# Performance work log

Measured on AMD Instinct MI355X. Metric: run time of the kernel, lower is better.

## Reference

```python
import jax, jax.numpy as jnp
import numpy as np

EPS = 1e-5
N = 384
CZ = 128  # pair channels (c_z)
CH = 128  # hidden channels (c_hidden)


def _layer_norm(x, w, b):
    m = jnp.mean(x, axis=-1, keepdims=True)
    v = jnp.mean(jnp.square(x - m), axis=-1, keepdims=True)
    return (x - m) * jax.lax.rsqrt(v + EPS) * w + b


def setup_inputs() -> dict:
    key = jax.random.key(0)
    ks = jax.random.split(key, 8)
    s = 0.02  # weight init scale
    return {
        "z": jax.random.normal(ks[0], (1, N, N, CZ), jnp.float32),
        "ln_in_w": jnp.ones((2, CZ), jnp.float32),
        "ln_in_b": jnp.zeros((2, CZ), jnp.float32),
        "w_ag": jax.random.normal(ks[1], (2, CZ, CH), jnp.float32) * s,
        "b_ag": jnp.zeros((2, CH), jnp.float32),
        "w_ap": jax.random.normal(ks[2], (2, CZ, CH), jnp.float32) * s,
        "b_ap": jnp.zeros((2, CH), jnp.float32),
        "w_bg": jax.random.normal(ks[3], (2, CZ, CH), jnp.float32) * s,
        "b_bg": jnp.zeros((2, CH), jnp.float32),
        "w_bp": jax.random.normal(ks[4], (2, CZ, CH), jnp.float32) * s,
        "b_bp": jnp.zeros((2, CH), jnp.float32),
        "ln_out_w": jnp.ones((2, CH), jnp.float32),
        "ln_out_b": jnp.zeros((2, CH), jnp.float32),
        "w_z": jax.random.normal(ks[5], (2, CH, CZ), jnp.float32) * s,
        "b_z": jnp.zeros((2, CZ), jnp.float32),
        "w_g": jax.random.normal(ks[6], (2, CZ, CZ), jnp.float32) * s,
        "b_g": jnp.zeros((2, CZ), jnp.float32),
    }


def _tri_mul(z, outgoing, ln_in_w, ln_in_b, w_ag, b_ag, w_ap, b_ap,
             w_bg, b_bg, w_bp, b_bp, ln_out_w, ln_out_b, w_z, b_z, w_g, b_g):
    zn = _layer_norm(z, ln_in_w, ln_in_b)                      # [1,N,N,CZ]
    a = jax.nn.sigmoid(zn @ w_ag + b_ag) * (zn @ w_ap + b_ap)  # [1,N,N,CH]
    b = jax.nn.sigmoid(zn @ w_bg + b_bg) * (zn @ w_bp + b_bp)  # [1,N,N,CH]
    if outgoing:
        # p[i,k,c] = sum_j a[i,j,c] * b[k,j,c]
        p = jnp.einsum('bijc,bkjc->bikc', a, b)
    else:
        # p[i,k,c] = sum_j a[j,i,c] * b[j,k,c]
        p = jnp.einsum('bjic,bjkc->bikc', a, b)
    p = _layer_norm(p, ln_out_w, ln_out_b) @ w_z + b_z         # [1,N,N,CZ]
    g = jax.nn.sigmoid(zn @ w_g + b_g)
    return p * g


def reference(z, ln_in_w, ln_in_b, w_ag, b_ag, w_ap, b_ap, w_bg, b_bg,
              w_bp, b_bp, ln_out_w, ln_out_b, w_z, b_z, w_g, b_g):
    # idx 0: TriMulOut (outgoing=True), idx 1: TriMulIn (outgoing=False)
    for idx, outgoing in enumerate((True, False)):
        z = z + _tri_mul(z, outgoing,
                         ln_in_w[idx], ln_in_b[idx],
                         w_ag[idx], b_ag[idx], w_ap[idx], b_ap[idx],
                         w_bg[idx], b_bg[idx], w_bp[idx], b_bp[idx],
                         ln_out_w[idx], ln_out_b[idx],
                         w_z[idx], b_z[idx], w_g[idx], b_g[idx])
    return z
```

## Files before the change

### kernel.cpp

```cpp
#include <hip/hip_runtime.h>


constexpr int NS = 384;
constexpr int NN = NS * NS;

using bf16x8 = __attribute__((ext_vector_type(8))) __bf16;
using f32x4  = __attribute__((ext_vector_type(4))) float;

__device__ inline void load16_to_lds(const __bf16* g, __bf16* lds) {
  auto* gp = reinterpret_cast<const __attribute__((address_space(1))) unsigned int*>(
      reinterpret_cast<uintptr_t>(g));
  auto* lp = reinterpret_cast<__attribute__((address_space(3))) unsigned int*>(
      reinterpret_cast<uintptr_t>(lds));
  __builtin_amdgcn_global_load_lds(gp, lp, 16, 0, 0);
}

__global__ __launch_bounds__(256) void prep_weights(
    const float* __restrict__ w_ag, const float* __restrict__ w_ap,
    const float* __restrict__ w_bg, const float* __restrict__ w_bp,
    const float* __restrict__ w_g,  const float* __restrict__ w_z,
    __bf16* __restrict__ wsw)
{
  int gid  = blockIdx.x * 256 + threadIdx.x;
  int mat  = gid >> 11;
  int slot = gid & 2047;
  int lane = slot & 63;
  int tb   = (slot >> 6) & 7;
  int s    = slot >> 9;
  int pass = mat / 6, which = mat % 6;
  const float* W;
  switch (which) {
    case 0: W = w_ag; break; case 1: W = w_ap; break; case 2: W = w_bg; break;
    case 3: W = w_bp; break; case 4: W = w_g;  break; default: W = w_z;
  }
  W += pass * 16384;
  int n0 = tb * 16 + (lane & 15);
  int k0 = s * 32 + (lane >> 4) * 8;
  __bf16* dst = wsw + ((size_t)mat * 2048 + slot) * 8;
#pragma unroll
  for (int j = 0; j < 8; ++j) dst[j] = (__bf16)W[(k0 + j) * 128 + n0];
}

__global__ __launch_bounds__(256) void proj_kernel(
    const float* __restrict__ zsrc, const float* __restrict__ lnw, const float* __restrict__ lnb,
    const __bf16* __restrict__ wsw5,
    const float* __restrict__ bag, const float* __restrict__ bap,
    const float* __restrict__ bbg, const float* __restrict__ bbp, const float* __restrict__ bgg,
    __bf16* __restrict__ a_t, __bf16* __restrict__ b_t, __bf16* __restrict__ g_out, int mode)
{
  __shared__ __bf16 zn[64][136];
  int tid = threadIdx.x;
  int rb = 0, r2 = 0;
  size_t pstart = 0;
  if (mode == 0) pstart = (size_t)blockIdx.x * 64;
  else { rb = blockIdx.x / NS; r2 = blockIdx.x % NS; }

  {
    int row = tid >> 2, q = tid & 3;
    size_t zoff = (mode == 0) ? (pstart + row) * 128
                              : ((size_t)(64 * rb + row) * NS + r2) * 128;
    const float4* zp = (const float4*)(zsrc + zoff) + q * 8;
    float4 v[8];
#pragma unroll
    for (int u = 0; u < 8; ++u) v[u] = zp[u];
    float s1 = 0.f, s2 = 0.f;
#pragma unroll
    for (int u = 0; u < 8; ++u) {
      float4 t = v[u];
      s1 += t.x + t.y + t.z + t.w;
      s2 += t.x * t.x + t.y * t.y + t.z * t.z + t.w * t.w;
    }
    s1 += __shfl_xor(s1, 1); s2 += __shfl_xor(s2, 1);
    s1 += __shfl_xor(s1, 2); s2 += __shfl_xor(s2, 2);
    float mean = s1 * (1.0f / 128.0f);
    float var  = s2 * (1.0f / 128.0f) - mean * mean;
    float rstd = rsqrtf(var + 1e-5f);
#pragma unroll
    for (int u = 0; u < 8; ++u) {
      int c0 = q * 32 + u * 4;
      float4 t  = v[u];
      float4 w4 = *(const float4*)(lnw + c0);
      float4 b4 = *(const float4*)(lnb + c0);
      zn[row][c0 + 0] = (__bf16)((t.x - mean) * rstd * w4.x + b4.x);
      zn[row][c0 + 1] = (__bf16)((t.y - mean) * rstd * w4.y + b4.y);
      zn[row][c0 + 2] = (__bf16)((t.z - mean) * rstd * w4.z + b4.z);
      zn[row][c0 + 3] = (__bf16)((t.w - mean) * rstd * w4.w + b4.w);
    }
  }
  __syncthreads();

  const int wv = tid >> 6;
  const int lane = tid & 63;
  const int lm = lane & 15;
  const int lq = lane >> 4;
  const size_t wposbase = (mode == 0) ? pstart : ((size_t)r2 * NS + 64 * rb);

  bf16x8 znf[4][4];
#pragma unroll
  for (int nt = 0; nt < 4; ++nt)
#pragma unroll
    for (int s = 0; s < 4; ++s)
      znf[nt][s] = *(const bf16x8*)(&zn[16 * nt + lm][32 * s + 8 * lq]);

#pragma unroll
  for (int grp = 0; grp < 3; ++grp) {
    const __bf16* wA;
    const __bf16* wB = nullptr;
    const float* pbA;
    const float* pbB = nullptr;
    __bf16* dst = nullptr;
    if (grp == 0)      { wA = wsw5;             wB = wsw5 + 16384;   pbA = bag; pbB = bap; dst = a_t; }
    else if (grp == 1) { wA = wsw5 + 2 * 16384; wB = wsw5 + 3 * 16384; pbA = bbg; pbB = bbp; dst = b_t; }
    else               { wA = wsw5 + 4 * 16384; pbA = bgg; }

#pragma unroll
    for (int mbi = 0; mbi < 2; ++mbi) {
      const int mb = 2 * wv + mbi;
      bf16x8 fA[4], fB[4];
#pragma unroll
      for (int s = 0; s < 4; ++s) {
        fA[s] = *(const bf16x8*)(wA + ((size_t)((s * 8 + mb) * 64 + lane)) * 8);
        if (grp < 2) fB[s] = *(const bf16x8*)(wB + ((size_t)((s * 8 + mb) * 64 + lane)) * 8);
      }
      if (grp < 2) {
        float biasA[4], biasB[4];
#pragma unroll
        for (int r = 0; r < 4; ++r) {
          int cc = 16 * mb + 4 * lq + r;
          biasA[r] = pbA[cc];
          biasB[r] = pbB[cc];
        }
#pragma unroll
        for (int nt = 0; nt < 4; ++nt) {
          f32x4 acc0 = {0.f, 0.f, 0.f, 0.f}, acc1 = {0.f, 0.f, 0.f, 0.f};
#pragma unroll
          for (int s = 0; s < 4; ++s) {
            acc0 = __builtin_amdgcn_mfma_f32_16x16x32_bf16(fA[s], znf[nt][s], acc0, 0, 0, 0);
            acc1 = __builtin_amdgcn_mfma_f32_16x16x32_bf16(fB[s], znf[nt][s], acc1, 0, 0, 0);
          }
          size_t wp = wposbase + 16 * nt + lm;
#pragma unroll
          for (int r = 0; r < 4; ++r) {
            int cc = 16 * mb + 4 * lq + r;
            float xg = acc0[r] + biasA[r];
            float xp = acc1[r] + biasB[r];
            float val = xp / (1.0f + __expf(-xg));
            dst[(size_t)cc * NN + wp] = (__bf16)val;
          }
        }
      } else {
        float biasG = pbA[16 * mb + lm];
#pragma unroll
        for (int nt = 0; nt < 4; ++nt) {
          f32x4 acc = {0.f, 0.f, 0.f, 0.f};
#pragma unroll
          for (int s = 0; s < 4; ++s)
            acc = __builtin_amdgcn_mfma_f32_16x16x32_bf16(znf[nt][s], fA[s], acc, 0, 0, 0);
          int cc = 16 * mb + lm;
#pragma unroll
          for (int r = 0; r < 4; ++r) {
            int pos = 16 * nt + 4 * lq + r;
            size_t gp = (mode == 0) ? (pstart + pos) * 128
                                    : ((size_t)(64 * rb + pos) * NS + r2) * 128;
            float val = 1.0f / (1.0f + __expf(-(acc[r] + biasG)));
            g_out[gp + cc] = (__bf16)val;
          }
        }
      }
    }
  }
}

__global__ __launch_bounds__(256) void tri_kernel(
    const __bf16* __restrict__ a_t, const __bf16* __restrict__ b_t, __bf16* __restrict__ p_t)
{
  __shared__ __bf16 As[128 * 64];
  __shared__ __bf16 Bs[128 * 64];
  int c  = blockIdx.z;
  int i0 = blockIdx.x * 128, k0 = blockIdx.y * 128;
  const __bf16* Ab = a_t + (size_t)c * NN;
  const __bf16* Bb = b_t + (size_t)c * NN;
  int tid = threadIdx.x, wv = tid >> 6, lane = tid & 63;
  int lm = lane & 15, lq = lane >> 4;
  int lrow = lane >> 3;
  int lsl  = lane & 7;
  int lch  = lsl ^ lrow;
  f32x4 acc[4][4];
#pragma unroll
  for (int mi = 0; mi < 4; ++mi)
#pragma unroll
    for (int ni = 0; ni < 4; ++ni) acc[mi][ni] = {0.f, 0.f, 0.f, 0.f};
  const int rowA_half = 64 * (wv & 1), colB_half = 64 * (wv >> 1);

  for (int kk = 0; kk < 384; kk += 64) {
    __syncthreads();
#pragma unroll
    for (int v = 0; v < 4; ++v) {
      int rgrp = 4 * wv + v;
      int r = 8 * rgrp + lrow;
      load16_to_lds(Ab + (size_t)(i0 + r) * NS + kk + lch * 8, As + rgrp * 512);
      load16_to_lds(Bb + (size_t)(k0 + r) * NS + kk + lch * 8, Bs + rgrp * 512);
    }
    __syncthreads();
#pragma unroll
    for (int s = 0; s < 2; ++s) {
      bf16x8 bfr[4], afr[4];
#pragma unroll
      for (int ni = 0; ni < 4; ++ni)
        bfr[ni] = *(const bf16x8*)(Bs + (colB_half + 16 * ni + lm) * 64 +
                                   ((4 * s + lq) ^ (lm & 7)) * 8);
#pragma unroll
      for (int mi = 0; mi < 4; ++mi)
        afr[mi] = *(const bf16x8*)(As + (rowA_half + 16 * mi + lm) * 64 +
                                   ((4 * s + lq) ^ (lm & 7)) * 8);
#pragma unroll
      for (int mi = 0; mi < 4; ++mi)
#pragma unroll
        for (int ni = 0; ni < 4; ++ni)
          acc[mi][ni] = __builtin_amdgcn_mfma_f32_16x16x32_bf16(afr[mi], bfr[ni], acc[mi][ni], 0, 0, 0);
    }
  }
#pragma unroll
  for (int mi = 0; mi < 4; ++mi)
#pragma unroll
    for (int ni = 0; ni < 4; ++ni)
#pragma unroll
      for (int r = 0; r < 4; ++r) {
        int row = i0 + rowA_half + 16 * mi + 4 * lq + r;
        int col = k0 + colB_half + 16 * ni + lm;
        p_t[(size_t)c * NN + (size_t)row * NS + col] = (__bf16)acc[mi][ni][r];
      }
}

__global__ __launch_bounds__(256) void out_kernel(
    const __bf16* __restrict__ p_t, const __bf16* __restrict__ g_in,
    const float* __restrict__ z_in, float* __restrict__ z_out,
    const float* __restrict__ lnw, const float* __restrict__ lnb,
    const __bf16* __restrict__ wz, const float* __restrict__ bz)
{
  __shared__ __bf16 pl[64][136];
  int tid = threadIdx.x;
  size_t base = (size_t)blockIdx.x * 64;

  {
    int c2 = tid >> 1, hf = tid & 1;
    const __bf16* src = p_t + (size_t)c2 * NN + base + hf * 32;
    bf16x8 v0 = ((const bf16x8*)src)[0];
    bf16x8 v1 = ((const bf16x8*)src)[1];
    bf16x8 v2 = ((const bf16x8*)src)[2];
    bf16x8 v3 = ((const bf16x8*)src)[3];
#pragma unroll
    for (int j = 0; j < 8; ++j) pl[hf * 32 + j][c2] = v0[j];
#pragma unroll
    for (int j = 0; j < 8; ++j) pl[hf * 32 + 8 + j][c2] = v1[j];
#pragma unroll
    for (int j = 0; j < 8; ++j) pl[hf * 32 + 16 + j][c2] = v2[j];
#pragma unroll
    for (int j = 0; j < 8; ++j) pl[hf * 32 + 24 + j][c2] = v3[j];
  }
  __syncthreads();

  {
    int row = tid >> 2, q = tid & 3;
    bf16x8 pv[4];
#pragma unroll
    for (int s = 0; s < 4; ++s) pv[s] = *(const bf16x8*)(&pl[row][q * 32 + 8 * s]);
    float s1 = 0.f, s2 = 0.f;
#pragma unroll
    for (int s = 0; s < 4; ++s)
#pragma unroll
      for (int j = 0; j < 8; ++j) { float f = (float)pv[s][j]; s1 += f; s2 += f * f; }
    s1 += __shfl_xor(s1, 1); s2 += __shfl_xor(s2, 1);
    s1 += __shfl_xor(s1, 2); s2 += __shfl_xor(s2, 2);
    float mean = s1 * (1.0f / 128.0f);
    float var  = s2 * (1.0f / 128.0f) - mean * mean;
    float rstd = rsqrtf(var + 1e-5f);
#pragma unroll
    for (int s = 0; s < 4; ++s) {
#pragma unroll
      for (int j = 0; j < 8; ++j) {
        int cc = q * 32 + 8 * s + j;
        float f = ((float)pv[s][j] - mean) * rstd * lnw[cc] + lnb[cc];
        pv[s][j] = (__bf16)f;
      }
      *(bf16x8*)(&pl[row][q * 32 + 8 * s]) = pv[s];
    }
  }
  __syncthreads();

  int wv = tid >> 6, lane = tid & 63, lm = lane & 15, lq = lane >> 4;
  bf16x8 wzf[2][4];
  float bzv[2];
#pragma unroll
  for (int nbi = 0; nbi < 2; ++nbi) {
    int nb = 2 * wv + nbi;
    bzv[nbi] = bz[16 * nb + lm];
#pragma unroll
    for (int s = 0; s < 4; ++s)
      wzf[nbi][s] = *(const bf16x8*)(wz + ((size_t)((s * 8 + nb) * 64 + lane)) * 8);
  }
#pragma unroll
  for (int mt = 0; mt < 4; ++mt) {
    bf16x8 af[4];
#pragma unroll
    for (int s = 0; s < 4; ++s)
      af[s] = *(const bf16x8*)(&pl[16 * mt + lm][32 * s + 8 * lq]);
#pragma unroll
    for (int nbi = 0; nbi < 2; ++nbi) {
      f32x4 acc = {0.f, 0.f, 0.f, 0.f};
#pragma unroll
      for (int s = 0; s < 4; ++s)
        acc = __builtin_amdgcn_mfma_f32_16x16x32_bf16(af[s], wzf[nbi][s], acc, 0, 0, 0);
      int cz = 16 * (2 * wv + nbi) + lm;
#pragma unroll
      for (int r = 0; r < 4; ++r) {
        int pos = 16 * mt + 4 * lq + r;
        size_t idx = (base + pos) * 128 + cz;
        float gv  = (float)g_in[idx];
        float res = (acc[r] + bzv[nbi]) * gv + z_in[idx];
        z_out[idx] = res;
      }
    }
  }
}

extern "C" void kernel_launch(void* const* d_in, const int* in_sizes, int n_in,
                              void* d_out, int out_size, void* d_ws, size_t ws_size,
                              hipStream_t stream) {
  (void)in_sizes; (void)n_in; (void)out_size; (void)ws_size;
  const float* z        = (const float*)d_in[0];
  const float* ln_in_w  = (const float*)d_in[1];
  const float* ln_in_b  = (const float*)d_in[2];
  const float* w_ag     = (const float*)d_in[3];
  const float* b_ag     = (const float*)d_in[4];
  const float* w_ap     = (const float*)d_in[5];
  const float* b_ap     = (const float*)d_in[6];
  const float* w_bg     = (const float*)d_in[7];
  const float* b_bg     = (const float*)d_in[8];
  const float* w_bp     = (const float*)d_in[9];
  const float* b_bp     = (const float*)d_in[10];
  const float* ln_out_w = (const float*)d_in[11];
  const float* ln_out_b = (const float*)d_in[12];
  const float* w_z      = (const float*)d_in[13];
  const float* b_z      = (const float*)d_in[14];
  const float* w_g      = (const float*)d_in[15];
  const float* b_g      = (const float*)d_in[16];
  float* out = (float*)d_out;

  __bf16* wsw = (__bf16*)d_ws;
  __bf16* a_t = wsw + 12 * 16384;
  __bf16* b_t = a_t + (size_t)NN * 128;
  __bf16* g_b = b_t + (size_t)NN * 128;
  __bf16* p_t = g_b + (size_t)NN * 128;

  prep_weights<<<96, 256, 0, stream>>>(w_ag, w_ap, w_bg, w_bp, w_g, w_z, wsw);

  for (int idx = 0; idx < 2; ++idx) {
    const float* zsrc = (idx == 0) ? z : out;
    const __bf16* wsw5 = wsw + (size_t)idx * 6 * 16384;
    proj_kernel<<<2304, 256, 0, stream>>>(
        zsrc, ln_in_w + idx * 128, ln_in_b + idx * 128, wsw5,
        b_ag + idx * 128, b_ap + idx * 128, b_bg + idx * 128, b_bp + idx * 128,
        b_g + idx * 128, a_t, b_t, g_b, idx);
    tri_kernel<<<dim3(3, 3, 128), 256, 0, stream>>>(a_t, b_t, p_t);
    out_kernel<<<2304, 256, 0, stream>>>(
        p_t, g_b, zsrc, out, ln_out_w + idx * 128, ln_out_b + idx * 128,
        wsw5 + 5 * 16384, b_z + idx * 128);
  }
}
```

Baseline: 461.4 us.

## Split input layernorm into own kernel and restage projection outputs through LDS

New measurement: 543.0 us. 1.18x slower.

```diff
diff --git a/kernel.cpp b/kernel.cpp
--- a/kernel.cpp
+++ b/kernel.cpp
@@ -13,6 +13,11 @@
   auto* lp = reinterpret_cast<__attribute__((address_space(3))) unsigned int*>(
       reinterpret_cast<uintptr_t>(lds));
   __builtin_amdgcn_global_load_lds(gp, lp, 16, 0, 0);
+}
+
+__device__ inline float sigmoidf_fast(float x) {
+  float e = __expf(-x);
+  return __builtin_amdgcn_rcpf(1.0f + e);
 }
 
 __global__ __launch_bounds__(256) void prep_weights(
@@ -41,132 +46,186 @@
   for (int j = 0; j < 8; ++j) dst[j] = (__bf16)W[(k0 + j) * 128 + n0];
 }
 
-__global__ __launch_bounds__(256) void proj_kernel(
+__global__ __launch_bounds__(256) void ln_kernel(
     const float* __restrict__ zsrc, const float* __restrict__ lnw, const float* __restrict__ lnb,
-    const __bf16* __restrict__ wsw5,
+    __bf16* __restrict__ zn, int mode)
+{
+  int tid = threadIdx.x;
+  int row = tid >> 2, q = tid & 3;
+  size_t zoff, qidx;
+  if (mode == 0) { qidx = (size_t)blockIdx.x * 64 + row; zoff = qidx * 128; }
+  else {
+    int i = blockIdx.x / 6;
+    int j = (blockIdx.x % 6) * 64 + row;
+    zoff = ((size_t)j * NS + i) * 128;
+    qidx = (size_t)i * NS + j;
+  }
+  const float4* zp = (const float4*)(zsrc + zoff) + q * 8;
+  float4 v[8];
+#pragma unroll
+  for (int u = 0; u < 8; ++u) v[u] = zp[u];
+  float s1 = 0.f, s2 = 0.f;
+#pragma unroll
+  for (int u = 0; u < 8; ++u) {
+    float4 t = v[u];
+    s1 += t.x + t.y + t.z + t.w;
+    s2 += t.x * t.x + t.y * t.y + t.z * t.z + t.w * t.w;
+  }
+  s1 += __shfl_xor(s1, 1); s2 += __shfl_xor(s2, 1);
+  s1 += __shfl_xor(s1, 2); s2 += __shfl_xor(s2, 2);
+  float mean = s1 * (1.0f / 128.0f);
+  float var  = s2 * (1.0f / 128.0f) - mean * mean;
+  float rstd = rsqrtf(var + 1e-5f);
+  bf16x8 o[4];
+#pragma unroll
+  for (int u = 0; u < 8; ++u) {
+    int c0 = q * 32 + u * 4;
+    float4 t  = v[u];
+    float4 w4 = *(const float4*)(lnw + c0);
+    float4 b4 = *(const float4*)(lnb + c0);
+    o[u >> 1][(u & 1) * 4 + 0] = (__bf16)((t.x - mean) * rstd * w4.x + b4.x);
+    o[u >> 1][(u & 1) * 4 + 1] = (__bf16)((t.y - mean) * rstd * w4.y + b4.y);
+    o[u >> 1][(u & 1) * 4 + 2] = (__bf16)((t.z - mean) * rstd * w4.z + b4.z);
+    o[u >> 1][(u & 1) * 4 + 3] = (__bf16)((t.w - mean) * rstd * w4.w + b4.w);
+  }
+  __bf16* dst = zn + qidx * 128 + q * 32;
+#pragma unroll
+  for (int u = 0; u < 4; ++u) *(bf16x8*)(dst + u * 8) = o[u];
+}
+
+__global__ __launch_bounds__(256, 2) void proj2_kernel(
+    const __bf16* __restrict__ zn, const __bf16* __restrict__ wsw5,
     const float* __restrict__ bag, const float* __restrict__ bap,
-    const float* __restrict__ bbg, const float* __restrict__ bbp, const float* __restrict__ bgg,
-    __bf16* __restrict__ a_t, __bf16* __restrict__ b_t, __bf16* __restrict__ g_out, int mode)
+    const float* __restrict__ bbg, const float* __restrict__ bbp,
+    const float* __restrict__ bgg,
+    __bf16* __restrict__ a_t, __bf16* __restrict__ b_t, __bf16* __restrict__ g_out,
+    int mode)
 {
-  __shared__ __bf16 zn[64][136];
-  int tid = threadIdx.x;
-  int rb = 0, r2 = 0;
-  size_t pstart = 0;
-  if (mode == 0) pstart = (size_t)blockIdx.x * 64;
-  else { rb = blockIdx.x / NS; r2 = blockIdx.x % NS; }
+  __shared__ __bf16 znlds[128 * 128];
+  __shared__ __bf16 alds[128 * 128];
+
+  const int tid = threadIdx.x;
+  const int wv = tid >> 6, lane = tid & 63;
+  const int lm = lane & 15, lq = lane >> 4;
+  const int prod = blockIdx.y;
+  const bool twomat = (prod != 2);
+  const __bf16* wbase = wsw5 + (size_t)prod * 2 * 16384;
+  const size_t pbase = (size_t)blockIdx.x * 128;
 
   {
-    int row = tid >> 2, q = tid & 3;
-    size_t zoff = (mode == 0) ? (pstart + row) * 128
-                              : ((size_t)(64 * rb + row) * NS + r2) * 128;
-    const float4* zp = (const float4*)(zsrc + zoff) + q * 8;
-    float4 v[8];
-#pragma unroll
-    for (int u = 0; u < 8; ++u) v[u] = zp[u];
-    float s1 = 0.f, s2 = 0.f;
-#pragma unroll
-    for (int u = 0; u < 8; ++u) {
-      float4 t = v[u];
-      s1 += t.x + t.y + t.z + t.w;
-      s2 += t.x * t.x + t.y * t.y + t.z * t.z + t.w * t.w;
-    }
-    s1 += __shfl_xor(s1, 1); s2 += __shfl_xor(s2, 1);
-    s1 += __shfl_xor(s1, 2); s2 += __shfl_xor(s2, 2);
-    float mean = s1 * (1.0f / 128.0f);
-    float var  = s2 * (1.0f / 128.0f) - mean * mean;
-    float rstd = rsqrtf(var + 1e-5f);
-#pragma unroll
-    for (int u = 0; u < 8; ++u) {
-      int c0 = q * 32 + u * 4;
-      float4 t  = v[u];
-      float4 w4 = *(const float4*)(lnw + c0);
-      float4 b4 = *(const float4*)(lnb + c0);
-      zn[row][c0 + 0] = (__bf16)((t.x - mean) * rstd * w4.x + b4.x);
-      zn[row][c0 + 1] = (__bf16)((t.y - mean) * rstd * w4.y + b4.y);
-      zn[row][c0 + 2] = (__bf16)((t.z - mean) * rstd * w4.z + b4.z);
-      zn[row][c0 + 3] = (__bf16)((t.w - mean) * rstd * w4.w + b4.w);
-    }
-  }
+    const __bf16* zsrc = zn + pbase * 128;
+    int lrow = lane >> 4, lsl = lane & 15;
+#pragma unroll
+    for (int t = 0; t < 8; ++t) {
+      int rbase = (wv * 8 + t) * 4;
+      int row = rbase + lrow;
+      int chunk = lsl ^ (row & 15);
+      load16_to_lds(zsrc + (size_t)row * 128 + chunk * 8, znlds + rbase * 128);
+    }
+  }
+
+  const int n0 = 2 * wv;
+  bf16x8 wf[2][2][4];
+#pragma unroll
+  for (int n2 = 0; n2 < 2; ++n2)
+#pragma unroll
+    for (int s = 0; s < 4; ++s) {
+      wf[n2][0][s] = *(const bf16x8*)(wbase + ((size_t)((s * 8 + n0 + n2) * 64 + lane)) * 8);
+      if (twomat)
+        wf[n2][1][s] = *(const bf16x8*)(wbase + 16384 + ((size_t)((s * 8 + n0 + n2) * 64 + lane)) * 8);
+    }
+  const float* pbA = (prod == 0) ? bag : (prod == 1) ? bbg : bgg;
+  const float* pbB = (prod == 0) ? bap : bbp;
+  float bA[2], bB[2];
+#pragma unroll
+  for (int n2 = 0; n2 < 2; ++n2) {
+    bA[n2] = pbA[(n0 + n2) * 16 + lm];
+    bB[n2] = twomat ? pbB[(n0 + n2) * 16 + lm] : 0.f;
+  }
+
+  f32x4 acc[8][2][2];
+#pragma unroll
+  for (int m = 0; m < 8; ++m)
+#pragma unroll
+    for (int n2 = 0; n2 < 2; ++n2)
+#pragma unroll
+      for (int mt = 0; mt < 2; ++mt) acc[m][n2][mt] = {0.f, 0.f, 0.f, 0.f};
+
   __syncthreads();
 
-  const int wv = tid >> 6;
-  const int lane = tid & 63;
-  const int lm = lane & 15;
-  const int lq = lane >> 4;
-  const size_t wposbase = (mode == 0) ? pstart : ((size_t)r2 * NS + 64 * rb);
-
-  bf16x8 znf[4][4];
-#pragma unroll
-  for (int nt = 0; nt < 4; ++nt)
+#pragma unroll
+  for (int m = 0; m < 8; ++m) {
+    bf16x8 zf[4];
+#pragma unroll
+    for (int s = 0; s < 4; ++s) {
+      int slot = (4 * s + lq) ^ lm;
+      zf[s] = *(const bf16x8*)(znlds + (m * 16 + lm) * 128 + slot * 8);
+    }
 #pragma unroll
     for (int s = 0; s < 4; ++s)
-      znf[nt][s] = *(const bf16x8*)(&zn[16 * nt + lm][32 * s + 8 * lq]);
-
-#pragma unroll
-  for (int grp = 0; grp < 3; ++grp) {
-    const __bf16* wA;
-    const __bf16* wB = nullptr;
-    const float* pbA;
-    const float* pbB = nullptr;
-    __bf16* dst = nullptr;
-    if (grp == 0)      { wA = wsw5;             wB = wsw5 + 16384;   pbA = bag; pbB = bap; dst = a_t; }
-    else if (grp == 1) { wA = wsw5 + 2 * 16384; wB = wsw5 + 3 * 16384; pbA = bbg; pbB = bbp; dst = b_t; }
-    else               { wA = wsw5 + 4 * 16384; pbA = bgg; }
-
-#pragma unroll
-    for (int mbi = 0; mbi < 2; ++mbi) {
-      const int mb = 2 * wv + mbi;
-      bf16x8 fA[4], fB[4];
-#pragma unroll
-      for (int s = 0; s < 4; ++s) {
-        fA[s] = *(const bf16x8*)(wA + ((size_t)((s * 8 + mb) * 64 + lane)) * 8);
-        if (grp < 2) fB[s] = *(const bf16x8*)(wB + ((size_t)((s * 8 + mb) * 64 + lane)) * 8);
-      }
-      if (grp < 2) {
-        float biasA[4], biasB[4];
+#pragma unroll
+      for (int n2 = 0; n2 < 2; ++n2) {
+        acc[m][n2][0] = __builtin_amdgcn_mfma_f32_16x16x32_bf16(zf[s], wf[n2][0][s], acc[m][n2][0], 0, 0, 0);
+        if (twomat)
+          acc[m][n2][1] = __builtin_amdgcn_mfma_f32_16x16x32_bf16(zf[s], wf[n2][1][s], acc[m][n2][1], 0, 0, 0);
+      }
+  }
+
+  if (prod < 2) {
+#pragma unroll
+    for (int m = 0; m < 8; ++m)
+#pragma unroll
+      for (int n2 = 0; n2 < 2; ++n2) {
+        int c = (n0 + n2) * 16 + lm;
+#pragma unroll
+        for (int rr = 0; rr < 2; ++rr) {
+          int pos = m * 16 + 4 * lq + 2 * rr;
+          float g0 = acc[m][n2][0][2 * rr]     + bA[n2];
+          float g1 = acc[m][n2][0][2 * rr + 1] + bA[n2];
+          float p0 = acc[m][n2][1][2 * rr]     + bB[n2];
+          float p1 = acc[m][n2][1][2 * rr + 1] + bB[n2];
+          union { __bf16 h[2]; unsigned u; } pk;
+          pk.h[0] = (__bf16)(p0 * sigmoidf_fast(g0));
+          pk.h[1] = (__bf16)(p1 * sigmoidf_fast(g1));
+          int addr = c * 128 + (((pos >> 3) ^ (c & 15)) << 3) + (pos & 7);
+          *(unsigned*)(&alds[addr]) = pk.u;
+        }
+      }
+    __syncthreads();
+    __bf16* outp = (prod == 0) ? a_t : b_t;
+    int c = tid & 127, half = tid >> 7;
+    __bf16* dst = outp + (size_t)c * NN + pbase;
+#pragma unroll
+    for (int jj = 0; jj < 8; ++jj) {
+      int j = half * 8 + jj;
+      bf16x8 vv = *(const bf16x8*)(&alds[c * 128 + ((j ^ (c & 15)) << 3)]);
+      *(bf16x8*)(dst + j * 8) = vv;
+    }
+  } else {
+#pragma unroll
+    for (int m = 0; m < 8; ++m)
+#pragma unroll
+      for (int n2 = 0; n2 < 2; ++n2) {
+        int c = (n0 + n2) * 16 + lm;
 #pragma unroll
         for (int r = 0; r < 4; ++r) {
-          int cc = 16 * mb + 4 * lq + r;
-          biasA[r] = pbA[cc];
-          biasB[r] = pbB[cc];
+          int pos = m * 16 + 4 * lq + r;
+          float gv = sigmoidf_fast(acc[m][n2][0][r] + bA[n2]);
+          int addr = pos * 128 + (((c >> 3) ^ (pos & 15)) << 3) + (c & 7);
+          alds[addr] = (__bf16)gv;
         }
-#pragma unroll
-        for (int nt = 0; nt < 4; ++nt) {
-          f32x4 acc0 = {0.f, 0.f, 0.f, 0.f}, acc1 = {0.f, 0.f, 0.f, 0.f};
-#pragma unroll
-          for (int s = 0; s < 4; ++s) {
-            acc0 = __builtin_amdgcn_mfma_f32_16x16x32_bf16(fA[s], znf[nt][s], acc0, 0, 0, 0);
-            acc1 = __builtin_amdgcn_mfma_f32_16x16x32_bf16(fB[s], znf[nt][s], acc1, 0, 0, 0);
-          }
-          size_t wp = wposbase + 16 * nt + lm;
-#pragma unroll
-          for (int r = 0; r < 4; ++r) {
-            int cc = 16 * mb + 4 * lq + r;
-            float xg = acc0[r] + biasA[r];
-            float xp = acc1[r] + biasB[r];
-            float val = xp / (1.0f + __expf(-xg));
-            dst[(size_t)cc * NN + wp] = (__bf16)val;
-          }
-        }
-      } else {
-        float biasG = pbA[16 * mb + lm];
-#pragma unroll
-        for (int nt = 0; nt < 4; ++nt) {
-          f32x4 acc = {0.f, 0.f, 0.f, 0.f};
-#pragma unroll
-          for (int s = 0; s < 4; ++s)
-            acc = __builtin_amdgcn_mfma_f32_16x16x32_bf16(znf[nt][s], fA[s], acc, 0, 0, 0);
-          int cc = 16 * mb + lm;
-#pragma unroll
-          for (int r = 0; r < 4; ++r) {
-            int pos = 16 * nt + 4 * lq + r;
-            size_t gp = (mode == 0) ? (pstart + pos) * 128
-                                    : ((size_t)(64 * rb + pos) * NS + r2) * 128;
-            float val = 1.0f / (1.0f + __expf(-(acc[r] + biasG)));
-            g_out[gp + cc] = (__bf16)val;
-          }
-        }
-      }
+      }
+    __syncthreads();
+    int pos = tid & 127, half = tid >> 7;
+    size_t q = pbase + pos;
+    size_t gp;
+    if (mode == 0) gp = q;
+    else { int i = (int)(q / NS); int j = (int)(q % NS); gp = (size_t)j * NS + i; }
+    __bf16* dst = g_out + gp * 128;
+#pragma unroll
+    for (int jj = 0; jj < 8; ++jj) {
+      int j = half * 8 + jj;
+      *(bf16x8*)(dst + j * 8) = *(const bf16x8*)(&alds[pos * 128 + ((j ^ (pos & 15)) << 3)]);
     }
   }
 }
@@ -347,24 +406,26 @@
   const float* b_g      = (const float*)d_in[16];
   float* out = (float*)d_out;
 
-  __bf16* wsw = (__bf16*)d_ws;
-  __bf16* a_t = wsw + 12 * 16384;
-  __bf16* b_t = a_t + (size_t)NN * 128;
-  __bf16* g_b = b_t + (size_t)NN * 128;
-  __bf16* p_t = g_b + (size_t)NN * 128;
+  __bf16* wsw  = (__bf16*)d_ws;
+  __bf16* a_t  = wsw + 12 * 16384;
+  __bf16* b_t  = a_t + (size_t)NN * 128;
+  __bf16* g_b  = b_t + (size_t)NN * 128;
+  __bf16* znpt = g_b + (size_t)NN * 128;
 
   prep_weights<<<96, 256, 0, stream>>>(w_ag, w_ap, w_bg, w_bp, w_g, w_z, wsw);
 
   for (int idx = 0; idx < 2; ++idx) {
     const float* zsrc = (idx == 0) ? z : out;
     const __bf16* wsw5 = wsw + (size_t)idx * 6 * 16384;
-    proj_kernel<<<2304, 256, 0, stream>>>(
-        zsrc, ln_in_w + idx * 128, ln_in_b + idx * 128, wsw5,
+    ln_kernel<<<2304, 256, 0, stream>>>(zsrc, ln_in_w + idx * 128, ln_in_b + idx * 128,
+                                        znpt, idx);
+    proj2_kernel<<<dim3(1152, 3), 256, 0, stream>>>(
+        znpt, wsw5,
         b_ag + idx * 128, b_ap + idx * 128, b_bg + idx * 128, b_bp + idx * 128,
         b_g + idx * 128, a_t, b_t, g_b, idx);
-    tri_kernel<<<dim3(3, 3, 128), 256, 0, stream>>>(a_t, b_t, p_t);
+    tri_kernel<<<dim3(3, 3, 128), 256, 0, stream>>>(a_t, b_t, znpt);
     out_kernel<<<2304, 256, 0, stream>>>(
-        p_t, g_b, zsrc, out, ln_out_w + idx * 128, ln_out_b + idx * 128,
+        znpt, g_b, zsrc, out, ln_out_w + idx * 128, ln_out_b + idx * 128,
         wsw5 + 5 * 16384, b_z + idx * 128);
   }
 }
```
